# Optimization experiments

Measured on AMD Instinct MI355X. Metric: run time of the kernel, lower is better.

Reference implementation:

```python
import jax, jax.numpy as jnp
import numpy as np

B = 4096
IND = 512
OUTD = 512
DEG = 2
P = 2  # dim_treat
KNOTS = [[0.33, 0.66], [0.33, 0.66]]
D = DEG + 1 + len(KNOTS[0])  # 5 basis functions per treatment dim


def setup_inputs() -> dict:
    key = jax.random.key(0)
    k1, k2, k3 = jax.random.split(key, 3)
    x = jax.random.uniform(k1, (B, P + IND), dtype=jnp.float32)  # treat dims in [0,1]
    weight = jax.random.uniform(k2, (IND, OUTD, D ** P), dtype=jnp.float32)  # torch.rand init
    bias = jax.random.uniform(k3, (OUTD, D ** P), dtype=jnp.float32)
    return {"x": x, "weight": weight, "bias": bias}


def _truncated_power_basis(x_treat):
    # x_treat: [B, P] -> basis: [B, P, D]
    knots = jnp.asarray(KNOTS, dtype=x_treat.dtype)  # [P, n_knots]
    # polynomial part: 1, x, x^2, ... x^DEG
    pows = jnp.stack([x_treat ** i for i in range(DEG + 1)], axis=-1)  # [B, P, DEG+1]
    # truncated part: relu(x - knot)^DEG  (DEG > 1 branch of original code)
    trunc = jax.nn.relu(x_treat[:, :, None] - knots[None, :, :]) ** DEG  # [B, P, n_knots]
    return jnp.concatenate([pows, trunc], axis=-1)


def reference(x, weight, bias):
    x_treat = x[:, :P]          # [B, P]
    x_feature = x[:, P:]        # [B, IND]
    basis = _truncated_power_basis(x_treat)  # [B, P, D]
    # Kronecker product across the two treatment dims: outer product, flattened
    kb = jnp.einsum('bi,bj->bij', basis[:, 0, :], basis[:, 1, :]).reshape(x.shape[0], D * P * 0 + D * D)  # [B, D^2]
    # fused: (weight^T @ x_feature) contracted with the per-sample basis coefficients
    out = jnp.einsum('bi,iod,bd->bo', x_feature, weight, kb)  # [B, OUTD]
    out = out + kb @ bias.T      # bias also varies with treatment basis
    out = jax.nn.relu(out)       # act='relu'
    # islastlayer=0: re-attach treatment dims
    return jnp.concatenate([x_treat, out], axis=1)  # [B, P + OUTD]
```

## Files before the change

kernel.cpp:

```cpp
#include <hip/hip_runtime.h>
#include <hip/hip_bf16.h>
#include <string.h>

#define NB    4096
#define IND_  512
#define OUTD_ 512
#define XCOLS 514
#define ND    25
#define KTOT  12800
#define KT2B  12928
#define NSPL  4

#define BM 256
#define BN 128
#define BKB 128

#define PWI 64
#define PWO 4
#define PWC (PWO * ND)
#define T8P 112

typedef float  f32x4  __attribute__((ext_vector_type(4)));
typedef int    i32x4  __attribute__((ext_vector_type(4)));
typedef int    i32x8  __attribute__((ext_vector_type(8)));
typedef unsigned short u16x4 __attribute__((ext_vector_type(4)));
typedef unsigned int   u32x2 __attribute__((ext_vector_type(2)));

__device__ __forceinline__ unsigned short f2bf(float f) {
  unsigned int x = __float_as_uint(f);
  return (unsigned short)((x + 0x7fffu + ((x >> 16) & 1u)) >> 16);
}

__device__ __forceinline__ float bf2f(unsigned short u) {
  return __uint_as_float(((unsigned int)u) << 16);
}

__device__ __forceinline__ unsigned int pk_bf16(float a, float b) {
  return (unsigned int)f2bf(a) | ((unsigned int)f2bf(b) << 16);
}

__device__ __forceinline__ unsigned char f2fp8(float v) {
  if (v < 0.015625f) {
    return (unsigned char)__float2int_rn(v * 512.0f);
  }
  unsigned int u = __float_as_uint(v);
  u += 0x7ffffu + ((u >> 20) & 1u);
  int e = (int)(u >> 23) - 127 + 7;
  unsigned int m = (u >> 20) & 7u;
  return (unsigned char)((e << 3) | m);
}

__device__ __forceinline__ float basis_f(float t, int j) {
  switch (j) {
    case 0: return 1.0f;
    case 1: return t;
    case 2: return t * t;
    case 3: { float r = t - 0.33f; r = r > 0.0f ? r : 0.0f; return r * r; }
    default:{ float r = t - 0.66f; r = r > 0.0f ? r : 0.0f; return r * r; }
  }
}

__device__ __forceinline__ void gload_lds16(const void* g, void* l) {
  __builtin_amdgcn_global_load_lds(
      (const __attribute__((address_space(1))) void*)g,
      (__attribute__((address_space(3))) void*)l, 16, 0, 0);
}

__device__ __forceinline__ void drain_all() {
  asm volatile("s_waitcnt vmcnt(0) lgkmcnt(0)" ::: "memory");
}

__global__ __launch_bounds__(256) void prep_all_kernel(
    const float* __restrict__ x, const float* __restrict__ W,
    const float* __restrict__ bias, unsigned char* __restrict__ Xf8,
    float* __restrict__ kb, unsigned char* __restrict__ kbT8,
    unsigned char* __restrict__ Wf8, float* __restrict__ out)
{
  __shared__ unsigned char tile8[PWI * T8P];
  const int bid = blockIdx.x;
  const int tid = threadIdx.x;

  if (bid < 512) {
    const int lane = tid & 63;
    #pragma unroll
    for (int rr = 0; rr < 2; ++rr) {
      const int b = bid * 8 + (tid >> 6) * 2 + rr;
      const float* xr = x + (size_t)b * XCOLS;
      const float* fp = xr + 2 + lane * 8;
      float2 a0 = *(const float2*)(fp + 0);
      float2 a1 = *(const float2*)(fp + 2);
      float2 a2 = *(const float2*)(fp + 4);
      float2 a3 = *(const float2*)(fp + 6);
      float xf[8] = {a0.x, a0.y, a1.x, a1.y, a2.x, a2.y, a3.x, a3.y};
      u32x2 pk;
      pk[0] = (unsigned int)f2fp8(xf[0]) | ((unsigned int)f2fp8(xf[1]) << 8) |
              ((unsigned int)f2fp8(xf[2]) << 16) | ((unsigned int)f2fp8(xf[3]) << 24);
      pk[1] = (unsigned int)f2fp8(xf[4]) | ((unsigned int)f2fp8(xf[5]) << 8) |
              ((unsigned int)f2fp8(xf[6]) << 16) | ((unsigned int)f2fp8(xf[7]) << 24);
      *reinterpret_cast<u32x2*>(Xf8 + (size_t)b * IND_ + lane * 8) = pk;

      float t0 = xr[0], t1 = xr[1];
      if (lane < 2) out[(size_t)b * XCOLS + lane] = (lane == 0) ? t0 : t1;
      {
        int d1 = lane / 5, d2 = lane - d1 * 5;
        float kv = basis_f(t0, d1) * basis_f(t1, d2);
        if (lane < ND) kb[(size_t)b * ND + lane] = kv;
      }
      {
        int ta = 2 * lane, tb = 2 * lane + 1;
        unsigned char ba = 0, bb = 0;
        if (ta < ND) { int d1 = ta / 5, d2 = ta - d1 * 5;
                       ba = f2fp8(basis_f(t0, d1) * basis_f(t1, d2)); }
        if (tb < ND) { int d1 = tb / 5, d2 = tb - d1 * 5;
                       bb = f2fp8(basis_f(t0, d1) * basis_f(t1, d2)); }
        *(unsigned short*)(kbT8 + (size_t)b * 128 + 2 * lane) =
            (unsigned short)ba | ((unsigned short)bb << 8);
      }
    }
  } else {
    const int pw = bid - 512;
    const int i0 = (pw & 7) * PWI;
    const int o0 = (pw >> 3) * PWO;

    for (int t = tid; t < PWI * (PWC / 4); t += 256) {
      int il = t / (PWC / 4);
      int c4 = t - il * (PWC / 4);
      float4 v = *(const float4*)(W + ((size_t)(i0 + il) * OUTD_ + o0) * ND + c4 * 4);
      unsigned int pk = (unsigned int)f2fp8(v.x) | ((unsigned int)f2fp8(v.y) << 8) |
                        ((unsigned int)f2fp8(v.z) << 16) | ((unsigned int)f2fp8(v.w) << 24);
      *(unsigned int*)&tile8[il * T8P + c4 * 4] = pk;
    }
    __syncthreads();

    for (int g = tid; g < PWC * (PWI / 8); g += 256) {
      int c  = g >> 3;
      int ig = g & 7;
      int d  = c % 25;
      int o_l = c / 25;
      unsigned long long v = 0;
      #pragma unroll
      for (int jj = 0; jj < 8; ++jj)
        v |= (unsigned long long)tile8[(ig * 8 + jj) * T8P + c] << (8 * jj);
      size_t rowb = (size_t)(o0 + o_l) * KT2B + (size_t)d * IND_ + i0;
      *reinterpret_cast<unsigned long long*>(Wf8 + rowb + ig * 8) = v;
    }

    if ((pw & 7) == 0) {
      int o = o0 + (tid >> 6);
      int p = tid & 63;
      int ta = 2 * p, tb = 2 * p + 1;
      unsigned char ba = (ta < ND) ? f2fp8(bias[o * ND + ta]) : (unsigned char)0;
      unsigned char bb = (tb < ND) ? f2fp8(bias[o * ND + tb]) : (unsigned char)0;
      *(unsigned short*)(Wf8 + (size_t)o * KT2B + KTOT + 2 * p) =
          (unsigned short)ba | ((unsigned short)bb << 8);
    }
  }
}

__global__ __launch_bounds__(512, 2) void gemm_mx_kernel(
    const unsigned char* __restrict__ Wf8, const unsigned char* __restrict__ Xf8,
    const float* __restrict__ kb, const unsigned char* __restrict__ kbT8,
    unsigned short* __restrict__ Pb)
{
  __shared__ unsigned char Als[2][BM * BKB];
  __shared__ unsigned char Bls[2][BN * BKB];

  const int tid  = threadIdx.x;
  const int lane = tid & 63;
  const int w    = tid >> 6;
  const int l15  = lane & 15;
  const int quad = lane >> 4;

  const int id  = blockIdx.x;
  const int xcd = id & 7;
  const int bx  = xcd & 1;
  const int bz  = xcd >> 1;
  const int by  = id >> 3;

  const int o0 = bx * BM;
  const int b0 = by * BN;
  const int ks_begin = bz * 3200;
  const bool tail = (bz == 3);

  const int o_off = (w & 3) * 64;
  const int b_off = (w >> 2) * 64;
  const int srow  = lane >> 3;
  const int scol  = ((lane & 7) ^ srow) * 16;
  const int r7    = l15 & 7;
  const int s0    = ((2 * quad) ^ r7) * 16;
  const int s1    = ((2 * quad + 1) ^ r7) * 16;

  const unsigned char* aRow[4];
  #pragma unroll
  for (int c = 0; c < 4; ++c)
    aRow[c] = Wf8 + (size_t)(o0 + (w * 4 + c) * 8 + srow) * KT2B + scol;
  const unsigned char* bRow[2];
  #pragma unroll
  for (int c = 0; c < 2; ++c)
    bRow[c] = Xf8 + (size_t)(b0 + (w * 2 + c) * 8 + srow) * IND_ + scol;
  const unsigned char* tRow[2];
  #pragma unroll
  for (int c = 0; c < 2; ++c)
    tRow[c] = kbT8 + (size_t)(b0 + (w * 2 + c) * 8 + srow) * 128 + scol;

  f32x4 acc[4][4], fin[4][4];
  #pragma unroll
  for (int i = 0; i < 4; ++i)
    #pragma unroll
    for (int jj = 0; jj < 4; ++jj) { acc[i][jj] = (f32x4)0.0f; fin[i][jj] = (f32x4)0.0f; }

  float kv[4] = {1.0f, 1.0f, 1.0f, 1.0f};
  int cur_d = -1;

  auto issueAB = [&](int ao, int bcol, int buf) {
    #pragma unroll
    for (int c = 0; c < 4; ++c)
      gload_lds16(aRow[c] + ao, &Als[buf][(w * 4 + c) * 1024]);
    #pragma unroll
    for (int c = 0; c < 2; ++c)
      gload_lds16(bRow[c] + bcol, &Bls[buf][(w * 2 + c) * 1024]);
  };

  int ao   = ks_begin;
  int bcol = ks_begin & 511;
  issueAB(ao, bcol, 0);
  drain_all();
  __syncthreads();

  for (int n = 0; n < 25; ++n) {
    const int p = n & 1;
    const int q = p ^ 1;

    if (n < 24) {
      ao += BKB;
      bcol = (bcol + BKB) & 511;
      issueAB(ao, bcol, q);
    } else if (tail) {
      #pragma unroll
      for (int c = 0; c < 4; ++c)
        gload_lds16(aRow[c] + KTOT, &Als[q][(w * 4 + c) * 1024]);
      #pragma unroll
      for (int c = 0; c < 2; ++c)
        gload_lds16(tRow[c], &Bls[q][(w * 2 + c) * 1024]);
    }

    const int d = (ks_begin + n * BKB) >> 9;
    if (d != cur_d) {
      if (cur_d >= 0) {
        #pragma unroll
        for (int nf = 0; nf < 4; ++nf)
          #pragma unroll
          for (int mf = 0; mf < 4; ++mf)
            #pragma unroll
            for (int r = 0; r < 4; ++r) {
              fin[mf][nf][r] += kv[nf] * acc[mf][nf][r];
              acc[mf][nf][r] = 0.0f;
            }
      }
      cur_d = d;
      #pragma unroll
      for (int nf = 0; nf < 4; ++nf)
        kv[nf] = kb[(size_t)(b0 + b_off + nf * 16 + l15) * ND + d];
    }

    {
      i32x8 af[4], bfr[4];
      #pragma unroll
      for (int mf = 0; mf < 4; ++mf) {
        int rb = (o_off + mf * 16 + l15) * BKB;
        i32x4 lo = *reinterpret_cast<const i32x4*>(&Als[p][rb + s0]);
        i32x4 hi = *reinterpret_cast<const i32x4*>(&Als[p][rb + s1]);
        i32x8 v;
        v[0] = lo[0]; v[1] = lo[1]; v[2] = lo[2]; v[3] = lo[3];
        v[4] = hi[0]; v[5] = hi[1]; v[6] = hi[2]; v[7] = hi[3];
        af[mf] = v;
      }
      #pragma unroll
      for (int nf = 0; nf < 4; ++nf) {
        int rb = (b_off + nf * 16 + l15) * BKB;
        i32x4 lo = *reinterpret_cast<const i32x4*>(&Bls[p][rb + s0]);
        i32x4 hi = *reinterpret_cast<const i32x4*>(&Bls[p][rb + s1]);
        i32x8 v;
        v[0] = lo[0]; v[1] = lo[1]; v[2] = lo[2]; v[3] = lo[3];
        v[4] = hi[0]; v[5] = hi[1]; v[6] = hi[2]; v[7] = hi[3];
        bfr[nf] = v;
      }
      #pragma unroll
      for (int mf = 0; mf < 4; ++mf)
        #pragma unroll
        for (int nf = 0; nf < 4; ++nf)
          acc[mf][nf] = __builtin_amdgcn_mfma_scale_f32_16x16x128_f8f6f4(
              af[mf], bfr[nf], acc[mf][nf],
              0, 0, 0, 0x7f7f7f7f, 0, 0x7f7f7f7f);
    }

    drain_all();
    __syncthreads();
  }

  #pragma unroll
  for (int nf = 0; nf < 4; ++nf)
    #pragma unroll
    for (int mf = 0; mf < 4; ++mf)
      #pragma unroll
      for (int r = 0; r < 4; ++r)
        fin[mf][nf][r] += kv[nf] * acc[mf][nf][r];

  if (tail) {
    i32x8 af[4], bfr[4];
    #pragma unroll
    for (int mf = 0; mf < 4; ++mf) {
      int rb = (o_off + mf * 16 + l15) * BKB;
      i32x4 lo = *reinterpret_cast<const i32x4*>(&Als[1][rb + s0]);
      i32x4 hi = *reinterpret_cast<const i32x4*>(&Als[1][rb + s1]);
      i32x8 v;
      v[0] = lo[0]; v[1] = lo[1]; v[2] = lo[2]; v[3] = lo[3];
      v[4] = hi[0]; v[5] = hi[1]; v[6] = hi[2]; v[7] = hi[3];
      af[mf] = v;
    }
    #pragma unroll
    for (int nf = 0; nf < 4; ++nf) {
      int rb = (b_off + nf * 16 + l15) * BKB;
      i32x4 lo = *reinterpret_cast<const i32x4*>(&Bls[1][rb + s0]);
      i32x4 hi = *reinterpret_cast<const i32x4*>(&Bls[1][rb + s1]);
      i32x8 v;
      v[0] = lo[0]; v[1] = lo[1]; v[2] = lo[2]; v[3] = lo[3];
      v[4] = hi[0]; v[5] = hi[1]; v[6] = hi[2]; v[7] = hi[3];
      bfr[nf] = v;
    }
    #pragma unroll
    for (int mf = 0; mf < 4; ++mf)
      #pragma unroll
      for (int nf = 0; nf < 4; ++nf)
        fin[mf][nf] = __builtin_amdgcn_mfma_scale_f32_16x16x128_f8f6f4(
            af[mf], bfr[nf], fin[mf][nf],
            0, 0, 0, 0x7f7f7f7f, 0, 0x7f7f7f7f);
  }

  unsigned short* Pz = Pb + (size_t)bz * NB * OUTD_;
  #pragma unroll
  for (int mf = 0; mf < 4; ++mf)
    #pragma unroll
    for (int nf = 0; nf < 4; ++nf) {
      int bg = b0 + b_off + nf * 16 + l15;
      int og = o0 + o_off + mf * 16 + quad * 4;
      u32x2 pk;
      pk[0] = pk_bf16(fin[mf][nf][0], fin[mf][nf][1]);
      pk[1] = pk_bf16(fin[mf][nf][2], fin[mf][nf][3]);
      *reinterpret_cast<u32x2*>(&Pz[(size_t)bg * OUTD_ + og]) = pk;
    }
}

__global__ __launch_bounds__(256) void epilogue_kernel(
    const unsigned short* __restrict__ Pb, float* __restrict__ out)
{
  const int idx = (blockIdx.x * 256 + threadIdx.x) * 4;
  const int b = idx >> 9;
  const int o = idx & 511;
  const size_t ps = (size_t)NB * OUTD_;
  float s[4] = {0.0f, 0.0f, 0.0f, 0.0f};
  #pragma unroll
  for (int z = 0; z < NSPL; ++z) {
    u16x4 v = *reinterpret_cast<const u16x4*>(&Pb[z * ps + idx]);
    #pragma unroll
    for (int e = 0; e < 4; ++e) s[e] += bf2f(v[e]);
  }
  float* op = out + (size_t)b * XCOLS + 2 + o;
  float2 lo, hi;
  lo.x = s[0] > 0.0f ? s[0] : 0.0f;
  lo.y = s[1] > 0.0f ? s[1] : 0.0f;
  hi.x = s[2] > 0.0f ? s[2] : 0.0f;
  hi.y = s[3] > 0.0f ? s[3] : 0.0f;
  *(float2*)op = lo;
  *(float2*)(op + 2) = hi;
}

extern "C" void kernel_launch(void* const* d_in, const int* in_sizes, int n_in,
                              void* d_out, int out_size, void* d_ws, size_t ws_size,
                              hipStream_t stream) {
  const float* x    = (const float*)d_in[0];
  const float* W    = (const float*)d_in[1];
  const float* bias = (const float*)d_in[2];
  float* out = (float*)d_out;
  char* ws = (char*)d_ws;

  const size_t xf_off  = 0;
  const size_t wf_off  = 2097152;
  const size_t kb_off  = wf_off + (size_t)OUTD_ * KT2B;
  const size_t kbt_off = kb_off + 409600;
  const size_t p_off   = kbt_off + (size_t)NB * 128;
  unsigned char* Xf8  = (unsigned char*)(ws + xf_off);
  unsigned char* Wf8  = (unsigned char*)(ws + wf_off);
  float* kb           = (float*)(ws + kb_off);
  unsigned char* kbT8 = (unsigned char*)(ws + kbt_off);
  unsigned short* Pb  = (unsigned short*)(ws + p_off);

  prep_all_kernel<<<1536, 256, 0, stream>>>(x, W, bias, Xf8, kb, kbT8, Wf8, out);
  gemm_mx_kernel<<<256, 512, 0, stream>>>(Wf8, Xf8, kb, kbT8, Pb);
  epilogue_kernel<<<(NB * OUTD_) / 1024, 256, 0, stream>>>(Pb, out);
}
```

Measured before the change: 130.3 us.

## Triple-buffer LDS pipeline with partial vmcnt waits in fp8 GEMM

Converts the double-buffered K loop into a three-stage LDS ring that prefetches two stages ahead and waits only for the oldest stage's loads instead of draining all memory counters each iteration. The bias/kb tail step is folded into the main loop as an extra iteration, and MFMA sections get raised wave priority. LDS use grows to 144KB per block, which likely no longer lets two 512-thread blocks share a CU, trading occupancy for deeper in-block latency hiding.

```diff
diff --git a/kernel.cpp b/kernel.cpp
--- a/kernel.cpp
+++ b/kernel.cpp
@@ -64,10 +64,6 @@
   __builtin_amdgcn_global_load_lds(
       (const __attribute__((address_space(1))) void*)g,
       (__attribute__((address_space(3))) void*)l, 16, 0, 0);
-}
-
-__device__ __forceinline__ void drain_all() {
-  asm volatile("s_waitcnt vmcnt(0) lgkmcnt(0)" ::: "memory");
 }
 
 __global__ __launch_bounds__(256) void prep_all_kernel(
@@ -162,8 +158,8 @@
     const float* __restrict__ kb, const unsigned char* __restrict__ kbT8,
     unsigned short* __restrict__ Pb)
 {
-  __shared__ unsigned char Als[2][BM * BKB];
-  __shared__ unsigned char Bls[2][BN * BKB];
+  __shared__ unsigned char Als[3][BM * BKB];
+  __shared__ unsigned char Bls[3][BN * BKB];
 
   const int tid  = threadIdx.x;
   const int lane = tid & 63;
@@ -181,6 +177,7 @@
   const int b0 = by * BN;
   const int ks_begin = bz * 3200;
   const bool tail = (bz == 3);
+  const int nIter = tail ? 26 : 25;
 
   const int o_off = (w & 3) * 64;
   const int b_off = (w >> 2) * 64;
@@ -212,39 +209,38 @@
   float kv[4] = {1.0f, 1.0f, 1.0f, 1.0f};
   int cur_d = -1;
 
-  auto issueAB = [&](int ao, int bcol, int buf) {
-    #pragma unroll
-    for (int c = 0; c < 4; ++c)
-      gload_lds16(aRow[c] + ao, &Als[buf][(w * 4 + c) * 1024]);
-    #pragma unroll
-    for (int c = 0; c < 2; ++c)
-      gload_lds16(bRow[c] + bcol, &Bls[buf][(w * 2 + c) * 1024]);
+  auto issue_for = [&](int m, int buf) {
+    if (m < 25) {
+      const int ao   = ks_begin + m * BKB;
+      const int bcol = ao & 511;
+      #pragma unroll
+      for (int c = 0; c < 4; ++c)
+        gload_lds16(aRow[c] + ao, &Als[buf][(w * 4 + c) * 1024]);
+      #pragma unroll
+      for (int c = 0; c < 2; ++c)
+        gload_lds16(bRow[c] + bcol, &Bls[buf][(w * 2 + c) * 1024]);
+    } else {
+      #pragma unroll
+      for (int c = 0; c < 4; ++c)
+        gload_lds16(aRow[c] + KTOT, &Als[buf][(w * 4 + c) * 1024]);
+      #pragma unroll
+      for (int c = 0; c < 2; ++c)
+        gload_lds16(tRow[c], &Bls[buf][(w * 2 + c) * 1024]);
+    }
   };
 
-  int ao   = ks_begin;
-  int bcol = ks_begin & 511;
-  issueAB(ao, bcol, 0);
-  drain_all();
-  __syncthreads();
-
-  for (int n = 0; n < 25; ++n) {
-    const int p = n & 1;
-    const int q = p ^ 1;
-
-    if (n < 24) {
-      ao += BKB;
-      bcol = (bcol + BKB) & 511;
-      issueAB(ao, bcol, q);
-    } else if (tail) {
-      #pragma unroll
-      for (int c = 0; c < 4; ++c)
-        gload_lds16(aRow[c] + KTOT, &Als[q][(w * 4 + c) * 1024]);
-      #pragma unroll
-      for (int c = 0; c < 2; ++c)
-        gload_lds16(tRow[c], &Bls[q][(w * 2 + c) * 1024]);
-    }
-
-    const int d = (ks_begin + n * BKB) >> 9;
+  issue_for(0, 0);
+  issue_for(1, 1);
+  asm volatile("s_waitcnt vmcnt(6)" ::: "memory");
+  __builtin_amdgcn_s_barrier();
+
+  int p = 0;
+  for (int n = 0; n < nIter; ++n) {
+    int q = p + 2; if (q >= 3) q -= 3;
+    const bool more2 = (n + 2 < nIter);
+    if (more2) issue_for(n + 2, q);
+
+    const int d = (n < 25) ? ((ks_begin + n * BKB) >> 9) : ND;
     if (d != cur_d) {
       if (cur_d >= 0) {
         #pragma unroll
@@ -258,11 +254,17 @@
             }
       }
       cur_d = d;
-      #pragma unroll
-      for (int nf = 0; nf < 4; ++nf)
-        kv[nf] = kb[(size_t)(b0 + b_off + nf * 16 + l15) * ND + d];
-    }
-
+      if (d < ND) {
+        #pragma unroll
+        for (int nf = 0; nf < 4; ++nf)
+          kv[nf] = kb[(size_t)(b0 + b_off + nf * 16 + l15) * ND + d];
+      } else {
+        #pragma unroll
+        for (int nf = 0; nf < 4; ++nf) kv[nf] = 1.0f;
+      }
+    }
+
+    __builtin_amdgcn_s_setprio(1);
     {
       i32x8 af[4], bfr[4];
       #pragma unroll
@@ -293,9 +295,17 @@
               af[mf], bfr[nf], acc[mf][nf],
               0, 0, 0, 0x7f7f7f7f, 0, 0x7f7f7f7f);
     }
-
-    drain_all();
-    __syncthreads();
+    __builtin_amdgcn_s_setprio(0);
+
+    if (n + 1 < nIter) {
+      if (more2) {
+        asm volatile("s_waitcnt vmcnt(6)" ::: "memory");
+      } else {
+        asm volatile("s_waitcnt vmcnt(0)" ::: "memory");
+      }
+      __builtin_amdgcn_s_barrier();
+    }
+    p = (p + 1 == 3) ? 0 : p + 1;
   }
 
   #pragma unroll
@@ -305,37 +315,6 @@
       #pragma unroll
       for (int r = 0; r < 4; ++r)
         fin[mf][nf][r] += kv[nf] * acc[mf][nf][r];
-
-  if (tail) {
-    i32x8 af[4], bfr[4];
-    #pragma unroll
-    for (int mf = 0; mf < 4; ++mf) {
-      int rb = (o_off + mf * 16 + l15) * BKB;
-      i32x4 lo = *reinterpret_cast<const i32x4*>(&Als[1][rb + s0]);
-      i32x4 hi = *reinterpret_cast<const i32x4*>(&Als[1][rb + s1]);
-      i32x8 v;
-      v[0] = lo[0]; v[1] = lo[1]; v[2] = lo[2]; v[3] = lo[3];
-      v[4] = hi[0]; v[5] = hi[1]; v[6] = hi[2]; v[7] = hi[3];
-      af[mf] = v;
-    }
-    #pragma unroll
-    for (int nf = 0; nf < 4; ++nf) {
-      int rb = (b_off + nf * 16 + l15) * BKB;
-      i32x4 lo = *reinterpret_cast<const i32x4*>(&Bls[1][rb + s0]);
-      i32x4 hi = *reinterpret_cast<const i32x4*>(&Bls[1][rb + s1]);
-      i32x8 v;
-      v[0] = lo[0]; v[1] = lo[1]; v[2] = lo[2]; v[3] = lo[3];
-      v[4] = hi[0]; v[5] = hi[1]; v[6] = hi[2]; v[7] = hi[3];
-      bfr[nf] = v;
-    }
-    #pragma unroll
-    for (int mf = 0; mf < 4; ++mf)
-      #pragma unroll
-      for (int nf = 0; nf < 4; ++nf)
-        fin[mf][nf] = __builtin_amdgcn_mfma_scale_f32_16x16x128_f8f6f4(
-            af[mf], bfr[nf], fin[mf][nf],
-            0, 0, 0, 0x7f7f7f7f, 0, 0x7f7f7f7f);
-  }
 
   unsigned short* Pz = Pb + (size_t)bz * NB * OUTD_;
   #pragma unroll
```

Result: slower. 133.5 us (+2.5%).

## Split K by input-feature slice so X tile stays in registers, triple-buffer W

Applied to the files above, without the earlier changes.

Each block now owns a fixed 128-wide slice of the input features across all 25 basis terms instead of a contiguous K range. The X fragment is loaded once into registers, and only W streams through a three-stage LDS ring with partial vmcnt waits. The basis weighting is applied each step with a telescoping difference (kv_cur - kv_next), so the per-basis accumulator never needs resetting. This cuts X reloads and full drains per step, but adds a per-iteration FMA over all accumulators and uses more LDS per block, which could reduce occupancy.

```diff
diff --git a/kernel.cpp b/kernel.cpp
--- a/kernel.cpp
+++ b/kernel.cpp
@@ -64,10 +64,6 @@
   __builtin_amdgcn_global_load_lds(
       (const __attribute__((address_space(1))) void*)g,
       (__attribute__((address_space(3))) void*)l, 16, 0, 0);
-}
-
-__device__ __forceinline__ void drain_all() {
-  asm volatile("s_waitcnt vmcnt(0) lgkmcnt(0)" ::: "memory");
 }
 
 __global__ __launch_bounds__(256) void prep_all_kernel(
@@ -162,8 +158,9 @@
     const float* __restrict__ kb, const unsigned char* __restrict__ kbT8,
     unsigned short* __restrict__ Pb)
 {
-  __shared__ unsigned char Als[2][BM * BKB];
-  __shared__ unsigned char Bls[2][BN * BKB];
+  __shared__ unsigned char Als[3][BM * BKB];
+  __shared__ unsigned char Bls[BN * BKB];
+  __shared__ unsigned char BTls[BN * BKB];
 
   const int tid  = threadIdx.x;
   const int lane = tid & 63;
@@ -172,15 +169,14 @@
   const int quad = lane >> 4;
 
   const int id  = blockIdx.x;
-  const int xcd = id & 7;
-  const int bx  = xcd & 1;
-  const int bz  = xcd >> 1;
+  const int bx  = id & 1;
+  const int iw  = (id >> 1) & 3;
   const int by  = id >> 3;
 
   const int o0 = bx * BM;
   const int b0 = by * BN;
-  const int ks_begin = bz * 3200;
-  const bool tail = (bz == 3);
+  const bool tail = (iw == 3);
+  const int lastA = tail ? 25 : 24;
 
   const int o_off = (w & 3) * 64;
   const int b_off = (w >> 2) * 64;
@@ -194,14 +190,43 @@
   #pragma unroll
   for (int c = 0; c < 4; ++c)
     aRow[c] = Wf8 + (size_t)(o0 + (w * 4 + c) * 8 + srow) * KT2B + scol;
-  const unsigned char* bRow[2];
+
+  auto issueA = [&](int m, int buf) {
+    const int ko = (m < 25) ? (m * 512 + iw * 128) : KTOT;
+    #pragma unroll
+    for (int c = 0; c < 4; ++c)
+      gload_lds16(aRow[c] + ko, &Als[buf][(w * 4 + c) * 1024]);
+  };
+
   #pragma unroll
   for (int c = 0; c < 2; ++c)
-    bRow[c] = Xf8 + (size_t)(b0 + (w * 2 + c) * 8 + srow) * IND_ + scol;
-  const unsigned char* tRow[2];
+    gload_lds16(kbT8 + (size_t)(b0 + (w * 2 + c) * 8 + srow) * 128 + scol,
+                &BTls[(w * 2 + c) * 1024]);
   #pragma unroll
   for (int c = 0; c < 2; ++c)
-    tRow[c] = kbT8 + (size_t)(b0 + (w * 2 + c) * 8 + srow) * 128 + scol;
+    gload_lds16(Xf8 + (size_t)(b0 + (w * 2 + c) * 8 + srow) * IND_ + iw * 128 + scol,
+                &Bls[(w * 2 + c) * 1024]);
+  issueA(0, 0);
+  issueA(1, 1);
+  asm volatile("s_waitcnt vmcnt(4)" ::: "memory");
+  __builtin_amdgcn_s_barrier();
+
+  i32x8 bfr[4];
+  #pragma unroll
+  for (int nf = 0; nf < 4; ++nf) {
+    int rb = (b_off + nf * 16 + l15) * BKB;
+    i32x4 lo = *reinterpret_cast<const i32x4*>(&Bls[rb + s0]);
+    i32x4 hi = *reinterpret_cast<const i32x4*>(&Bls[rb + s1]);
+    i32x8 v;
+    v[0] = lo[0]; v[1] = lo[1]; v[2] = lo[2]; v[3] = lo[3];
+    v[4] = hi[0]; v[5] = hi[1]; v[6] = hi[2]; v[7] = hi[3];
+    bfr[nf] = v;
+  }
+
+  const float* kvB = kb + (size_t)(b0 + b_off + l15) * ND;
+  float kvc[4];
+  #pragma unroll
+  for (int nf = 0; nf < 4; ++nf) kvc[nf] = kvB[nf * 16 * ND + 0];
 
   f32x4 acc[4][4], fin[4][4];
   #pragma unroll
@@ -209,62 +234,22 @@
     #pragma unroll
     for (int jj = 0; jj < 4; ++jj) { acc[i][jj] = (f32x4)0.0f; fin[i][jj] = (f32x4)0.0f; }
 
-  float kv[4] = {1.0f, 1.0f, 1.0f, 1.0f};
-  int cur_d = -1;
-
-  auto issueAB = [&](int ao, int bcol, int buf) {
-    #pragma unroll
-    for (int c = 0; c < 4; ++c)
-      gload_lds16(aRow[c] + ao, &Als[buf][(w * 4 + c) * 1024]);
-    #pragma unroll
-    for (int c = 0; c < 2; ++c)
-      gload_lds16(bRow[c] + bcol, &Bls[buf][(w * 2 + c) * 1024]);
-  };
-
-  int ao   = ks_begin;
-  int bcol = ks_begin & 511;
-  issueAB(ao, bcol, 0);
-  drain_all();
-  __syncthreads();
-
+  int p = 0;
   for (int n = 0; n < 25; ++n) {
-    const int p = n & 1;
-    const int q = p ^ 1;
-
+    const int m = n + 2;
+    if (m <= lastA) issueA(m, m % 3);
+
+    float kvn[4];
     if (n < 24) {
-      ao += BKB;
-      bcol = (bcol + BKB) & 511;
-      issueAB(ao, bcol, q);
-    } else if (tail) {
-      #pragma unroll
-      for (int c = 0; c < 4; ++c)
-        gload_lds16(aRow[c] + KTOT, &Als[q][(w * 4 + c) * 1024]);
-      #pragma unroll
-      for (int c = 0; c < 2; ++c)
-        gload_lds16(tRow[c], &Bls[q][(w * 2 + c) * 1024]);
-    }
-
-    const int d = (ks_begin + n * BKB) >> 9;
-    if (d != cur_d) {
-      if (cur_d >= 0) {
-        #pragma unroll
-        for (int nf = 0; nf < 4; ++nf)
-          #pragma unroll
-          for (int mf = 0; mf < 4; ++mf)
-            #pragma unroll
-            for (int r = 0; r < 4; ++r) {
-              fin[mf][nf][r] += kv[nf] * acc[mf][nf][r];
-              acc[mf][nf][r] = 0.0f;
-            }
-      }
-      cur_d = d;
-      #pragma unroll
-      for (int nf = 0; nf < 4; ++nf)
-        kv[nf] = kb[(size_t)(b0 + b_off + nf * 16 + l15) * ND + d];
+      #pragma unroll
+      for (int nf = 0; nf < 4; ++nf) kvn[nf] = kvB[nf * 16 * ND + (n + 1)];
+    } else {
+      #pragma unroll
+      for (int nf = 0; nf < 4; ++nf) kvn[nf] = 0.0f;
     }
 
     {
-      i32x8 af[4], bfr[4];
+      i32x8 af[4];
       #pragma unroll
       for (int mf = 0; mf < 4; ++mf) {
         int rb = (o_off + mf * 16 + l15) * BKB;
@@ -276,16 +261,6 @@
         af[mf] = v;
       }
       #pragma unroll
-      for (int nf = 0; nf < 4; ++nf) {
-        int rb = (b_off + nf * 16 + l15) * BKB;
-        i32x4 lo = *reinterpret_cast<const i32x4*>(&Bls[p][rb + s0]);
-        i32x4 hi = *reinterpret_cast<const i32x4*>(&Bls[p][rb + s1]);
-        i32x8 v;
-        v[0] = lo[0]; v[1] = lo[1]; v[2] = lo[2]; v[3] = lo[3];
-        v[4] = hi[0]; v[5] = hi[1]; v[6] = hi[2]; v[7] = hi[3];
-        bfr[nf] = v;
-      }
-      #pragma unroll
       for (int mf = 0; mf < 4; ++mf)
         #pragma unroll
         for (int nf = 0; nf < 4; ++nf)
@@ -294,20 +269,32 @@
               0, 0, 0, 0x7f7f7f7f, 0, 0x7f7f7f7f);
     }
 
-    drain_all();
-    __syncthreads();
-  }
-
-  #pragma unroll
-  for (int nf = 0; nf < 4; ++nf)
-    #pragma unroll
-    for (int mf = 0; mf < 4; ++mf)
-      #pragma unroll
-      for (int r = 0; r < 4; ++r)
-        fin[mf][nf][r] += kv[nf] * acc[mf][nf][r];
+    {
+      float dk[4];
+      #pragma unroll
+      for (int nf = 0; nf < 4; ++nf) dk[nf] = kvc[nf] - kvn[nf];
+      #pragma unroll
+      for (int mf = 0; mf < 4; ++mf)
+        #pragma unroll
+        for (int nf = 0; nf < 4; ++nf)
+          #pragma unroll
+          for (int r = 0; r < 4; ++r)
+            fin[mf][nf][r] += dk[nf] * acc[mf][nf][r];
+      #pragma unroll
+      for (int nf = 0; nf < 4; ++nf) kvc[nf] = kvn[nf];
+    }
+
+    if (n < 23) {
+      asm volatile("s_waitcnt vmcnt(8)" ::: "memory");
+    } else {
+      asm volatile("s_waitcnt vmcnt(0)" ::: "memory");
+    }
+    if (n < 24 || tail) __builtin_amdgcn_s_barrier();
+    p = (p + 1 == 3) ? 0 : p + 1;
+  }
 
   if (tail) {
-    i32x8 af[4], bfr[4];
+    i32x8 af[4], bft[4];
     #pragma unroll
     for (int mf = 0; mf < 4; ++mf) {
       int rb = (o_off + mf * 16 + l15) * BKB;
@@ -321,23 +308,23 @@
     #pragma unroll
     for (int nf = 0; nf < 4; ++nf) {
       int rb = (b_off + nf * 16 + l15) * BKB;
-      i32x4 lo = *reinterpret_cast<const i32x4*>(&Bls[1][rb + s0]);
-      i32x4 hi = *reinterpret_cast<const i32x4*>(&Bls[1][rb + s1]);
+      i32x4 lo = *reinterpret_cast<const i32x4*>(&BTls[rb + s0]);
+      i32x4 hi = *reinterpret_cast<const i32x4*>(&BTls[rb + s1]);
       i32x8 v;
       v[0] = lo[0]; v[1] = lo[1]; v[2] = lo[2]; v[3] = lo[3];
       v[4] = hi[0]; v[5] = hi[1]; v[6] = hi[2]; v[7] = hi[3];
-      bfr[nf] = v;
+      bft[nf] = v;
     }
     #pragma unroll
     for (int mf = 0; mf < 4; ++mf)
       #pragma unroll
       for (int nf = 0; nf < 4; ++nf)
         fin[mf][nf] = __builtin_amdgcn_mfma_scale_f32_16x16x128_f8f6f4(
-            af[mf], bfr[nf], fin[mf][nf],
+            af[mf], bft[nf], fin[mf][nf],
             0, 0, 0, 0x7f7f7f7f, 0, 0x7f7f7f7f);
   }
 
-  unsigned short* Pz = Pb + (size_t)bz * NB * OUTD_;
+  unsigned short* Pz = Pb + (size_t)iw * NB * OUTD_;
   #pragma unroll
   for (int mf = 0; mf < 4; ++mf)
     #pragma unroll
```

After: 126.8 us. 1.03x faster.
